# Optimization experiments

Hardware: AMD Instinct MI355X
Metric: run time of the kernel (lower is better)

## Reference

```python
import jax, jax.numpy as jnp
import numpy as np

B, T, HID = 2, 2048, 2048
H, KVH, D = 16, 4, 128
N_REP = H // KVH


def _rotate_half(x):
    x1, x2 = jnp.split(x, 2, axis=-1)
    return jnp.concatenate([-x2, x1], axis=-1)


def setup_inputs() -> dict:
    key = jax.random.key(0)
    ks = jax.random.split(key, 8)
    hidden_states = jax.random.normal(ks[0], (B, T, HID), dtype=jnp.float32)
    # RoPE tables: standard theta=10000 frequencies, emb = cat(freqs, freqs)
    inv_freq = 1.0 / (10000.0 ** (np.arange(0, D, 2, dtype=np.float32) / D))
    pos = np.arange(T, dtype=np.float32)
    freqs = np.outer(pos, inv_freq)                      # [T, D/2]
    emb = np.concatenate([freqs, freqs], axis=-1)        # [T, D]
    cos = jnp.broadcast_to(jnp.cos(emb)[None], (B, T, D)).astype(jnp.float32)
    sin = jnp.broadcast_to(jnp.sin(emb)[None], (B, T, D)).astype(jnp.float32)
    # causal additive mask [1,1,T,T]
    neg = jnp.finfo(jnp.float32).min
    causal = jnp.where(jnp.tril(jnp.ones((T, T), dtype=bool)), 0.0, neg)
    attention_mask = causal[None, None].astype(jnp.float32)
    s = 0.02
    Wq = jax.random.normal(ks[1], (H * D, HID), dtype=jnp.float32) * s
    Wk = jax.random.normal(ks[2], (KVH * D, HID), dtype=jnp.float32) * s
    Wv = jax.random.normal(ks[3], (KVH * D, HID), dtype=jnp.float32) * s
    Wo = jax.random.normal(ks[4], (HID, H * D), dtype=jnp.float32) * s
    bq = jnp.zeros((H * D,), dtype=jnp.float32)
    bk = jnp.zeros((KVH * D,), dtype=jnp.float32)
    bv = jnp.zeros((KVH * D,), dtype=jnp.float32)
    return {"hidden_states": hidden_states, "cos": cos, "sin": sin,
            "attention_mask": attention_mask,
            "Wq": Wq, "bq": bq, "Wk": Wk, "bk": bk, "Wv": Wv, "bv": bv, "Wo": Wo}


def reference(hidden_states, cos, sin, attention_mask, Wq, bq, Wk, bk, Wv, bv, Wo):
    bsz, q_len, _ = hidden_states.shape
    q = (jnp.einsum('bth,oh->bto', hidden_states, Wq) + bq).reshape(bsz, q_len, H, D).transpose(0, 2, 1, 3)
    k = (jnp.einsum('bth,oh->bto', hidden_states, Wk) + bk).reshape(bsz, q_len, KVH, D).transpose(0, 2, 1, 3)
    v = (jnp.einsum('bth,oh->bto', hidden_states, Wv) + bv).reshape(bsz, q_len, KVH, D).transpose(0, 2, 1, 3)
    c = cos[:, None, :, :]  # [B,1,T,D]
    s = sin[:, None, :, :]
    q = q * c + _rotate_half(q) * s
    k = k * c + _rotate_half(k) * s
    # repeat KV heads to match Q heads (GQA)
    k = jnp.repeat(k, N_REP, axis=1)  # [B,H,T,D]
    v = jnp.repeat(v, N_REP, axis=1)
    scores = jnp.einsum('bhqd,bhkd->bhqk', q, k) / jnp.sqrt(jnp.float32(D))
    scores = scores + attention_mask
    attn = jax.nn.softmax(scores.astype(jnp.float32), axis=-1).astype(q.dtype)
    out = jnp.einsum('bhqk,bhkd->bhqd', attn, v)          # [B,H,T,D]
    out = out.transpose(0, 2, 1, 3).reshape(bsz, q_len, H * D)
    return jnp.einsum('bto,ho->bth', out, Wo)
```

## Files before the change

kernel.cpp:

```cpp
#include <hip/hip_runtime.h>
#include <hip/hip_bf16.h>
#include <stdint.h>

#define B_ 2
#define T_ 2048
#define HID_ 2048
#define H_ 16
#define KVH_ 4
#define D_ 128

typedef __attribute__((ext_vector_type(8))) short short8;
typedef __attribute__((ext_vector_type(4))) float f32x4;

__device__ __forceinline__ uint16_t f2bf(float x) {
  union { float f; uint32_t u; } c; c.f = x;
  uint32_t r = c.u + 0x7fffu + ((c.u >> 16) & 1u);
  return (uint16_t)(r >> 16);
}
__device__ __forceinline__ float bf2f(uint16_t b) {
  union { uint32_t u; float f; } c; c.u = ((uint32_t)b) << 16;
  return c.f;
}
__device__ __forceinline__ uint16_t hwbf(float x) {
  __hip_bfloat16 h = __float2bfloat16(x);
  return *reinterpret_cast<uint16_t*>(&h);
}

#define XM(r) (((r) & 7) ^ (((r) >> 1) & 4))
#define SC_Q 0.1275523865396698f

__global__ __launch_bounds__(256) void cvt_all(const float* __restrict__ hidden,
                                               const float* __restrict__ Wq,
                                               const float* __restrict__ Wk,
                                               const float* __restrict__ Wv,
                                               const float* __restrict__ Wo,
                                               const float* __restrict__ bq,
                                               const float* __restrict__ bk,
                                               const float* __restrict__ bv,
                                               uint16_t* __restrict__ hidb,
                                               uint16_t* __restrict__ wqkv,
                                               uint16_t* __restrict__ wob,
                                               float* __restrict__ biasq) {
  const int gtid = blockIdx.x * 256 + threadIdx.x;
  const int i = gtid * 4;
  const float* src;
  uint16_t* dst;
  if (i < 8388608)       { src = hidden + i;            dst = hidb + i; }
  else if (i < 12582912) { src = Wq + (i - 8388608);    dst = wqkv + (i - 8388608); }
  else if (i < 13631488) { src = Wk + (i - 12582912);   dst = wqkv + 4194304 + (i - 12582912); }
  else if (i < 14680064) { src = Wv + (i - 13631488);   dst = wqkv + 5242880 + (i - 13631488); }
  else                   { src = Wo + (i - 14680064);   dst = wob + (i - 14680064); }
  const float4 v = *reinterpret_cast<const float4*>(src);
  union { uint16_t s[4]; uint2 u; } pk;
  pk.s[0] = f2bf(v.x); pk.s[1] = f2bf(v.y); pk.s[2] = f2bf(v.z); pk.s[3] = f2bf(v.w);
  *reinterpret_cast<uint2*>(dst) = pk.u;
  if (gtid < 3072)
    biasq[gtid] = (gtid < 2048) ? bq[gtid] : (gtid < 2560) ? bk[gtid - 2048] : bv[gtid - 2560];
}

#define QBM 256
#define QBN 256
#define BK 64

__global__ __launch_bounds__(512, 2) void gemm_qkv(const uint16_t* __restrict__ A,
                                                   const uint16_t* __restrict__ Bt,
                                                   const float* __restrict__ bias,
                                                   const float* __restrict__ cosp,
                                                   const float* __restrict__ sinp,
                                                   uint16_t* __restrict__ Qo,
                                                   uint16_t* __restrict__ Ko,
                                                   uint16_t* __restrict__ VtG) {
  __shared__ __align__(16) uint16_t Al[2][QBM * BK];
  __shared__ __align__(16) uint16_t Bl[2][QBN * BK];
  const int K = 2048;
  const int tid = threadIdx.x;
  const int w = tid >> 6;
  const int lane = tid & 63;
  const int wr = w >> 2, wc = w & 3;
  const int lm = lane & 15, lg = lane >> 4;

  const int orig = blockIdx.y * gridDim.x + blockIdx.x;
  const int xcd = orig & 7;
  const int cc = orig >> 3;
  const int bm = ((xcd & 3) * 4 + (cc & 3)) * QBM;
  const int bn = ((xcd >> 2) * 6 + (cc >> 2)) * QBN;

  const int cb0 = (wc >> 1) * 128 + (wc & 1) * 32;
  const int colb[4] = {cb0, cb0 + 16, cb0 + 64, cb0 + 80};

  f32x4 acc[8][4];
  const f32x4 z4 = {0.f, 0.f, 0.f, 0.f};
#pragma unroll
  for (int i = 0; i < 8; ++i)
#pragma unroll
    for (int j = 0; j < 4; ++j) acc[i][j] = z4;

  const int nt = K >> 6;

  auto stage = [&](int b, int t) {
    const int k0 = t * BK;
#pragma unroll
    for (int it = 0; it < 4; ++it) {
      const int chunk = it * 512 + tid;
      const int r = chunk >> 3, c8 = chunk & 7;
      const int csw = (c8 ^ XM(r)) * 8;
      const uint16_t* gA = A + (size_t)(bm + r) * K + k0 + csw;
      const uint16_t* gB = Bt + (size_t)(bn + r) * K + k0 + csw;
      __builtin_amdgcn_global_load_lds((const __attribute__((address_space(1))) unsigned int*)gA,
                                       (__attribute__((address_space(3))) unsigned int*)(&Al[b][0] + chunk * 8),
                                       16, 0, 0);
      __builtin_amdgcn_global_load_lds((const __attribute__((address_space(1))) unsigned int*)gB,
                                       (__attribute__((address_space(3))) unsigned int*)(&Bl[b][0] + chunk * 8),
                                       16, 0, 0);
    }
  };

  stage(0, 0);
  __syncthreads();

  int cur = 0;
  for (int t = 0; t < nt; ++t) {
    if (t + 1 < nt) stage(cur ^ 1, t + 1);
#pragma unroll
    for (int kk = 0; kk < 2; ++kk) {
      short8 bfr[4];
#pragma unroll
      for (int ni = 0; ni < 4; ++ni) {
        const int rb = colb[ni] + lm;
        bfr[ni] = *reinterpret_cast<const short8*>(&Bl[cur][rb * BK + (((kk * 4 + lg) ^ XM(rb)) * 8)]);
      }
#pragma unroll
      for (int mi = 0; mi < 8; ++mi) {
        const int r = wr * 128 + mi * 16 + lm;
        const short8 af = *reinterpret_cast<const short8*>(&Al[cur][r * BK + (((kk * 4 + lg) ^ XM(r)) * 8)]);
#pragma unroll
        for (int ni = 0; ni < 4; ++ni)
          acc[mi][ni] = __builtin_amdgcn_mfma_f32_16x16x32_bf16(af, bfr[ni], acc[mi][ni], 0, 0, 0);
      }
    }
    __syncthreads();
    cur ^= 1;
  }

  float bb[4];
#pragma unroll
  for (int ni = 0; ni < 4; ++ni) bb[ni] = bias[bn + colb[ni] + lm];

  if (bn < 2560) {
    const bool isQ = (bn < 2048);
    const int head0 = (isQ ? (bn >> 7) : ((bn - 2048) >> 7)) + (wc >> 1);
    const int nh = isQ ? H_ : KVH_;
    uint16_t* dst = isQ ? Qo : Ko;
    const float sc = isQ ? SC_Q : 1.0f;
#pragma unroll
    for (int mi = 0; mi < 8; ++mi) {
#pragma unroll
      for (int r = 0; r < 4; ++r) {
        const int row = bm + wr * 128 + mi * 16 + lg * 4 + r;
        const int b = row >> 11, tt = row & 2047;
        const float* cr = cosp + ((size_t)b * T_ + tt) * D_;
        const float* sr = sinp + ((size_t)b * T_ + tt) * D_;
        uint16_t* drow = dst + (((size_t)(b * nh + head0)) * T_ + tt) * D_;
#pragma unroll
        for (int ni = 0; ni < 4; ++ni) {
          const int d = (wc & 1) * 32 + (ni & 1) * 16 + (ni >> 1) * 64 + lm;
          const float xv = acc[mi][ni][r] + bb[ni];
          const float pv = acc[mi][ni ^ 2][r] + bb[ni ^ 2];
          const float sgn = (ni < 2) ? -1.f : 1.f;
          drow[d] = f2bf((xv * cr[d] + sgn * pv * sr[d]) * sc);
        }
      }
    }
  } else {
    const int kvh = ((bn - 2560) >> 7) + (wc >> 1);
#pragma unroll
    for (int mi = 0; mi < 8; ++mi) {
      const int row0 = bm + wr * 128 + mi * 16 + lg * 4;
      const int b = row0 >> 11, t0 = row0 & 2047;
#pragma unroll
      for (int ni = 0; ni < 4; ++ni) {
        const int d = (wc & 1) * 32 + (ni & 1) * 16 + (ni >> 1) * 64 + lm;
        union { uint16_t s[4]; uint2 u; } pk;
#pragma unroll
        for (int r = 0; r < 4; ++r) pk.s[r] = f2bf(acc[mi][ni][r] + bb[ni]);
        *reinterpret_cast<uint2*>(VtG + ((size_t)(b * KVH_ + kvh) * D_ + d) * T_ + t0) = pk.u;
      }
    }
  }
}

#define BM 128
#define BN 128

__global__ __launch_bounds__(512, 4) void gemm_bt(const uint16_t* __restrict__ A,
                                                  const uint16_t* __restrict__ Bt,
                                                  float* __restrict__ Cv,
                                                  int M, int N, int K) {
  __shared__ __align__(16) uint16_t Al[2][BM * BK];
  __shared__ __align__(16) uint16_t Bl[2][BN * BK];
  const int tid = threadIdx.x;
  const int w = tid >> 6;
  const int lane = tid & 63;
  const int wr = w >> 1, wc = w & 1;
  const int lm = lane & 15, lg = lane >> 4;

  const int GX = gridDim.x;
  const int orig = blockIdx.y * GX + blockIdx.x;
  const int xcd = orig & 7;
  const int cc = orig >> 3;
  const int bm = ((xcd >> 1) * 8 + (cc & 7)) * BM;
  const int bn = ((xcd & 1) * (GX >> 1) + (cc >> 3)) * BN;

  f32x4 acc[2][4];
  const f32x4 z4 = {0.f, 0.f, 0.f, 0.f};
#pragma unroll
  for (int i = 0; i < 2; ++i)
#pragma unroll
    for (int j = 0; j < 4; ++j) acc[i][j] = z4;

  const int nt = K >> 6;

  auto stage = [&](int b, int t) {
    const int k0 = t * BK;
#pragma unroll
    for (int it = 0; it < 2; ++it) {
      const int chunk = it * 512 + tid;
      const int r = chunk >> 3, c8 = chunk & 7;
      const int csw = (c8 ^ XM(r)) * 8;
      const uint16_t* gA = A + (size_t)(bm + r) * K + k0 + csw;
      const uint16_t* gB = Bt + (size_t)(bn + r) * K + k0 + csw;
      __builtin_amdgcn_global_load_lds((const __attribute__((address_space(1))) unsigned int*)gA,
                                       (__attribute__((address_space(3))) unsigned int*)(&Al[b][0] + chunk * 8),
                                       16, 0, 0);
      __builtin_amdgcn_global_load_lds((const __attribute__((address_space(1))) unsigned int*)gB,
                                       (__attribute__((address_space(3))) unsigned int*)(&Bl[b][0] + chunk * 8),
                                       16, 0, 0);
    }
  };

  stage(0, 0);
  __syncthreads();

  int cur = 0;
  for (int t = 0; t < nt; ++t) {
    if (t + 1 < nt) stage(cur ^ 1, t + 1);
#pragma unroll
    for (int kk = 0; kk < 2; ++kk) {
      short8 af[2], bfr[4];
#pragma unroll
      for (int mi = 0; mi < 2; ++mi) {
        const int r = wr * 32 + mi * 16 + lm;
        af[mi] = *reinterpret_cast<const short8*>(&Al[cur][r * BK + (((kk * 4 + lg) ^ XM(r)) * 8)]);
      }
#pragma unroll
      for (int ni = 0; ni < 4; ++ni) {
        const int r = wc * 64 + ni * 16 + lm;
        bfr[ni] = *reinterpret_cast<const short8*>(&Bl[cur][r * BK + (((kk * 4 + lg) ^ XM(r)) * 8)]);
      }
#pragma unroll
      for (int mi = 0; mi < 2; ++mi)
#pragma unroll
        for (int ni = 0; ni < 4; ++ni)
          acc[mi][ni] = __builtin_amdgcn_mfma_f32_16x16x32_bf16(af[mi], bfr[ni], acc[mi][ni], 0, 0, 0);
    }
    __syncthreads();
    cur ^= 1;
  }

#pragma unroll
  for (int mi = 0; mi < 2; ++mi) {
#pragma unroll
    for (int ni = 0; ni < 4; ++ni) {
      const int col = bn + wc * 64 + ni * 16 + lm;
#pragma unroll
      for (int r = 0; r < 4; ++r) {
        const int row = bm + wr * 32 + mi * 16 + lg * 4 + r;
        Cv[(size_t)row * N + col] = acc[mi][ni][r];
      }
    }
  }
}

#define KVBLK 64

__global__ __launch_bounds__(256, 2) void attn_fwd(const uint16_t* __restrict__ Qb,
                                                   const uint16_t* __restrict__ Kb,
                                                   const uint16_t* __restrict__ VtG,
                                                   uint16_t* __restrict__ Ab) {
  __shared__ __align__(16) uint16_t Kl[2][KVBLK * D_];
  __shared__ __align__(16) uint16_t Vtl[2][D_ * KVBLK];
  __shared__ __align__(16) uint16_t Pl[4 * 16 * 64];
  const int tid = threadIdx.x;
  const int w = tid >> 6, lane = tid & 63;
  const int lm = lane & 15, lg = lane >> 4;
  const int bh = blockIdx.y;
  const int b = bh >> 4, h = bh & 15;
  const int kvh = h >> 2;
  const int qtA = (blockIdx.x + bh) & 15;
  const int qtB = 31 - qtA;
  const int nA = qtA + 1;
  const int ntot = 33;

  const uint16_t* Kbase = Kb + ((size_t)(b * KVH_ + kvh)) * T_ * D_;
  const uint16_t* Vtbase = VtG + ((size_t)(b * KVH_ + kvh)) * D_ * T_;
  uint16_t* Pw = Pl + w * 16 * 64;
  const f32x4 z4 = {0.f, 0.f, 0.f, 0.f};

  short8 vone;
#pragma unroll
  for (int j = 0; j < 8; ++j) vone[j] = (short)0x3F80;

  f32x4 o[8];
  f32x4 osum;
  float mrow[4];
  short8 qf[4];

  auto loadQ = [&](int qt) {
    const uint16_t* Qw = Qb + (((size_t)(b * H_ + h)) * T_ + qt * 64 + w * 16) * D_;
#pragma unroll
    for (int kk = 0; kk < 4; ++kk)
      qf[kk] = *reinterpret_cast<const short8*>(Qw + (size_t)lm * D_ + kk * 32 + lg * 8);
  };
  auto resetAcc = [&]() {
#pragma unroll
    for (int f = 0; f < 8; ++f) o[f] = z4;
    osum = z4;
#pragma unroll
    for (int r = 0; r < 4; ++r) mrow[r] = -1e30f;
  };
  auto flush = [&](int qt) {
    const int wr0 = qt * 64 + w * 16;
    float rcp[4];
#pragma unroll
    for (int r = 0; r < 4; ++r) rcp[r] = 1.0f / osum[r];
#pragma unroll
    for (int f = 0; f < 8; ++f) {
      const int col = h * D_ + f * 16 + lm;
#pragma unroll
      for (int r = 0; r < 4; ++r) {
        const int trow = wr0 + lg * 4 + r;
        Ab[((size_t)(b * T_ + trow)) * (H_ * D_) + col] = f2bf(o[f][r] * rcp[r]);
      }
    }
  };
  auto stage = [&](int buf, int kv0) {
#pragma unroll
    for (int it = 0; it < 4; ++it) {
      const int chunk = it * 256 + tid;
      {
        const int r = chunk >> 4, c16 = chunk & 15;
        const uint16_t* g = Kbase + (size_t)(kv0 + r) * D_ + ((c16 ^ XM(r)) * 8);
        __builtin_amdgcn_global_load_lds((const __attribute__((address_space(1))) unsigned int*)g,
                                         (__attribute__((address_space(3))) unsigned int*)(&Kl[buf][0] + (it * 256 + w * 64) * 8),
                                         16, 0, 0);
      }
      {
        const int dd = chunk >> 3, c8 = chunk & 7;
        const uint16_t* g = Vtbase + (size_t)dd * T_ + kv0 + ((c8 ^ XM(dd)) * 8);
        __builtin_amdgcn_global_load_lds((const __attribute__((address_space(1))) unsigned int*)g,
                                         (__attribute__((address_space(3))) unsigned int*)(&Vtl[buf][0] + (it * 256 + w * 64) * 8),
                                         16, 0, 0);
      }
    }
  };

  loadQ(qtA);
  resetAcc();
  stage(0, 0);
  __syncthreads();

  int cur = 0;
  for (int g = 0; g < ntot; ++g) {
    const bool inA = g < nA;
    const int t = inA ? g : g - nA;
    const int qt = inA ? qtA : qtB;
    const int kv0 = t * KVBLK;
    const int wrow0 = qt * 64 + w * 16;

    if (g + 1 < ntot) {
      const int gn = g + 1;
      const int kvn = (gn < nA ? gn : gn - nA) * KVBLK;
      stage(cur ^ 1, kvn);
    }

    f32x4 s[4];
#pragma unroll
    for (int nf = 0; nf < 4; ++nf) s[nf] = z4;
#pragma unroll
    for (int nf = 0; nf < 4; ++nf)
#pragma unroll
      for (int kk = 0; kk < 4; ++kk) {
        const int row = nf * 16 + lm;
        const short8 kf = *reinterpret_cast<const short8*>(&Kl[cur][row * D_ + (((kk * 4 + lg) ^ XM(row)) * 8)]);
        s[nf] = __builtin_amdgcn_mfma_f32_16x16x32_bf16(qf[kk], kf, s[nf], 0, 0, 0);
      }

    if (kv0 + KVBLK - 1 > wrow0) {
#pragma unroll
      for (int nf = 0; nf < 4; ++nf) {
        const int colg = kv0 + nf * 16 + lm;
#pragma unroll
        for (int r = 0; r < 4; ++r) {
          const int rowg = wrow0 + lg * 4 + r;
          if (colg > rowg) s[nf][r] = -1e30f;
        }
      }
    }

    float tmax[4];
#pragma unroll
    for (int r = 0; r < 4; ++r)
      tmax[r] = fmaxf(fmaxf(s[0][r], s[1][r]), fmaxf(s[2][r], s[3][r]));
    bool grow = false;
#pragma unroll
    for (int r = 0; r < 4; ++r) grow = grow || (tmax[r] > mrow[r] + 8.f);
    if (__any((int)grow)) {
#pragma unroll
      for (int r = 0; r < 4; ++r) {
        float v = tmax[r];
        v = fmaxf(v, __shfl_xor(v, 1));
        v = fmaxf(v, __shfl_xor(v, 2));
        v = fmaxf(v, __shfl_xor(v, 4));
        v = fmaxf(v, __shfl_xor(v, 8));
        const float nm = fmaxf(mrow[r], v);
        const float al = exp2f(mrow[r] - nm);
        mrow[r] = nm;
        osum[r] *= al;
#pragma unroll
        for (int f = 0; f < 8; ++f) o[f][r] *= al;
      }
    }
#pragma unroll
    for (int nf = 0; nf < 4; ++nf)
#pragma unroll
      for (int r = 0; r < 4; ++r) {
        const float p = exp2f(s[nf][r] - mrow[r]);
        const int prow = lg * 4 + r;
        const int pchunk = (nf * 2 + (lm >> 3)) ^ XM(prow);
        Pw[prow * 64 + pchunk * 8 + (lm & 7)] = hwbf(p);
      }
    asm volatile("s_waitcnt lgkmcnt(0)" ::: "memory");
    short8 pf[2];
#pragma unroll
    for (int ks = 0; ks < 2; ++ks)
      pf[ks] = *reinterpret_cast<const short8*>(Pw + lm * 64 + (((ks * 4 + lg) ^ XM(lm)) * 8));
#pragma unroll
    for (int ks = 0; ks < 2; ++ks)
      osum = __builtin_amdgcn_mfma_f32_16x16x32_bf16(pf[ks], vone, osum, 0, 0, 0);
#pragma unroll
    for (int f = 0; f < 8; ++f)
#pragma unroll
      for (int ks = 0; ks < 2; ++ks) {
        const int dd = f * 16 + lm;
        const short8 vf = *reinterpret_cast<const short8*>(&Vtl[cur][dd * KVBLK + (((ks * 4 + lg) ^ XM(dd)) * 8)]);
        o[f] = __builtin_amdgcn_mfma_f32_16x16x32_bf16(pf[ks], vf, o[f], 0, 0, 0);
      }

    __syncthreads();
    cur ^= 1;

    if (g == nA - 1) {
      flush(qtA);
      loadQ(qtB);
      resetAcc();
    }
  }
  flush(qtB);
}

extern "C" void kernel_launch(void* const* d_in, const int* in_sizes, int n_in,
                              void* d_out, int out_size, void* d_ws, size_t ws_size,
                              hipStream_t stream) {
  const float* hidden = (const float*)d_in[0];
  const float* cosp   = (const float*)d_in[1];
  const float* sinp   = (const float*)d_in[2];
  const float* Wq = (const float*)d_in[4];
  const float* bq = (const float*)d_in[5];
  const float* Wk = (const float*)d_in[6];
  const float* bk = (const float*)d_in[7];
  const float* Wv = (const float*)d_in[8];
  const float* bv = (const float*)d_in[9];
  const float* Wo = (const float*)d_in[10];

  char* ws = (char*)d_ws;
  uint16_t* hidb   = (uint16_t*)(ws);
  uint16_t* wqkv   = (uint16_t*)(ws + 16777216);
  uint16_t* wob    = (uint16_t*)(ws + 29360128);
  float*    biasq  = (float*)   (ws + 37748736);
  uint16_t* Qb     = (uint16_t*)(ws + 62926848);
  uint16_t* Kb     = (uint16_t*)(ws + 79704064);
  uint16_t* VtG    = (uint16_t*)(ws + 83898368);
  uint16_t* Ab     = (uint16_t*)(ws + 88092672);

  cvt_all<<<18432, 256, 0, stream>>>(hidden, Wq, Wk, Wv, Wo, bq, bk, bv,
                                     hidb, wqkv, wob, biasq);
  gemm_qkv<<<dim3(12, 16), 512, 0, stream>>>(hidb, wqkv, biasq, cosp, sinp, Qb, Kb, VtG);
  attn_fwd<<<dim3(16, 32), 256, 0, stream>>>(Qb, Kb, VtG, Ab);
  gemm_bt<<<dim3(16, 32), 512, 0, stream>>>(Ab, wob, (float*)d_out, 4096, 2048, 2048);
}
```

Measured before the change: 200.3 us.

## Restructure QKV GEMM into 8-phase quadrant pipeline with half-tile staged loads

```diff
diff --git a/kernel.cpp b/kernel.cpp
--- a/kernel.cpp
+++ b/kernel.cpp
@@ -76,7 +76,7 @@
   const int tid = threadIdx.x;
   const int w = tid >> 6;
   const int lane = tid & 63;
-  const int wr = w >> 2, wc = w & 3;
+  const int wr = w >> 1, wc = w & 1;
   const int lm = lane & 15, lg = lane >> 4;
 
   const int orig = blockIdx.y * gridDim.x + blockIdx.x;
@@ -85,105 +85,153 @@
   const int bm = ((xcd & 3) * 4 + (cc & 3)) * QBM;
   const int bn = ((xcd >> 2) * 6 + (cc >> 2)) * QBN;
 
-  const int cb0 = (wc >> 1) * 128 + (wc & 1) * 32;
-  const int colb[4] = {cb0, cb0 + 16, cb0 + 64, cb0 + 80};
-
-  f32x4 acc[8][4];
+  f32x4 acc[4][2][4];
   const f32x4 z4 = {0.f, 0.f, 0.f, 0.f};
 #pragma unroll
-  for (int i = 0; i < 8; ++i)
-#pragma unroll
-    for (int j = 0; j < 4; ++j) acc[i][j] = z4;
-
-  const int nt = K >> 6;
-
-  auto stage = [&](int b, int t) {
+  for (int q = 0; q < 4; ++q)
+#pragma unroll
+    for (int mi = 0; mi < 2; ++mi)
+#pragma unroll
+      for (int ni = 0; ni < 4; ++ni) acc[q][mi][ni] = z4;
+
+  auto stage_half = [&](int buf, int t, int mat, int hh) {
     const int k0 = t * BK;
 #pragma unroll
-    for (int it = 0; it < 4; ++it) {
+    for (int it = 0; it < 2; ++it) {
       const int chunk = it * 512 + tid;
       const int r = chunk >> 3, c8 = chunk & 7;
-      const int csw = (c8 ^ XM(r)) * 8;
-      const uint16_t* gA = A + (size_t)(bm + r) * K + k0 + csw;
-      const uint16_t* gB = Bt + (size_t)(bn + r) * K + k0 + csw;
-      __builtin_amdgcn_global_load_lds((const __attribute__((address_space(1))) unsigned int*)gA,
-                                       (__attribute__((address_space(3))) unsigned int*)(&Al[b][0] + chunk * 8),
+      const int rr = hh * 128 + r;
+      const int csw = (c8 ^ XM(rr)) * 8;
+      const uint16_t* g = (mat == 0) ? (A + (size_t)(bm + rr) * K + k0 + csw)
+                                     : (Bt + (size_t)(bn + rr) * K + k0 + csw);
+      uint16_t* lb = (mat == 0) ? &Al[buf][0] : &Bl[buf][0];
+      __builtin_amdgcn_global_load_lds((const __attribute__((address_space(1))) unsigned int*)g,
+                                       (__attribute__((address_space(3))) unsigned int*)(lb + (size_t)rr * BK + c8 * 8),
                                        16, 0, 0);
-      __builtin_amdgcn_global_load_lds((const __attribute__((address_space(1))) unsigned int*)gB,
-                                       (__attribute__((address_space(3))) unsigned int*)(&Bl[b][0] + chunk * 8),
-                                       16, 0, 0);
     }
   };
 
-  stage(0, 0);
-  __syncthreads();
-
-  int cur = 0;
-  for (int t = 0; t < nt; ++t) {
-    if (t + 1 < nt) stage(cur ^ 1, t + 1);
-#pragma unroll
-    for (int kk = 0; kk < 2; ++kk) {
-      short8 bfr[4];
-#pragma unroll
-      for (int ni = 0; ni < 4; ++ni) {
-        const int rb = colb[ni] + lm;
-        bfr[ni] = *reinterpret_cast<const short8*>(&Bl[cur][rb * BK + (((kk * 4 + lg) ^ XM(rb)) * 8)]);
-      }
-#pragma unroll
-      for (int mi = 0; mi < 8; ++mi) {
-        const int r = wr * 128 + mi * 16 + lm;
-        const short8 af = *reinterpret_cast<const short8*>(&Al[cur][r * BK + (((kk * 4 + lg) ^ XM(r)) * 8)]);
-#pragma unroll
-        for (int ni = 0; ni < 4; ++ni)
-          acc[mi][ni] = __builtin_amdgcn_mfma_f32_16x16x32_bf16(af, bfr[ni], acc[mi][ni], 0, 0, 0);
-      }
-    }
-    __syncthreads();
-    cur ^= 1;
+  stage_half(0, 0, 1, 0);
+  stage_half(0, 0, 0, 0);
+  stage_half(0, 0, 0, 1);
+  stage_half(0, 0, 1, 1);
+  stage_half(1, 1, 1, 0);
+  stage_half(1, 1, 0, 0);
+  asm volatile("s_waitcnt vmcnt(8)" ::: "memory");
+  __builtin_amdgcn_s_barrier();
+
+  const int nIter = 16;
+  for (int i = 0; i < nIter; ++i) {
+    const bool lastIt = (i == nIter - 1);
+#pragma unroll
+    for (int p = 0; p < 8; ++p) {
+      const int bufc = p >> 2;
+      const int q = p & 3;
+      const int mh = q & 1, nh = q >> 1;
+      short8 af[2][2], bf[4][2];
+#pragma unroll
+      for (int mi = 0; mi < 2; ++mi)
+#pragma unroll
+        for (int kk = 0; kk < 2; ++kk) {
+          const int row = mh * 128 + wr * 32 + mi * 16 + lm;
+          af[mi][kk] = *reinterpret_cast<const short8*>(&Al[bufc][(size_t)row * BK + (((kk * 4 + lg) ^ XM(row)) * 8)]);
+        }
+#pragma unroll
+      for (int ni = 0; ni < 4; ++ni)
+#pragma unroll
+        for (int kk = 0; kk < 2; ++kk) {
+          const int row = nh * 128 + wc * 32 + (ni & 1) * 16 + (ni >> 1) * 64 + lm;
+          bf[ni][kk] = *reinterpret_cast<const short8*>(&Bl[bufc][(size_t)row * BK + (((kk * 4 + lg) ^ XM(row)) * 8)]);
+        }
+      if (p == 0)      stage_half(1, 2 * i + 1, 0, 1);
+      else if (p == 1) stage_half(1, 2 * i + 1, 1, 1);
+      else if (!lastIt) {
+        if (p == 2)      stage_half(0, 2 * i + 2, 1, 0);
+        else if (p == 3) stage_half(0, 2 * i + 2, 0, 0);
+        else if (p == 4) stage_half(0, 2 * i + 2, 0, 1);
+        else if (p == 5) stage_half(0, 2 * i + 2, 1, 1);
+        else if (p == 6) stage_half(1, 2 * i + 3, 1, 0);
+        else             stage_half(1, 2 * i + 3, 0, 0);
+      }
+      __builtin_amdgcn_s_barrier();
+      asm volatile("s_waitcnt lgkmcnt(0)" ::: "memory");
+      __builtin_amdgcn_sched_barrier(0);
+      __builtin_amdgcn_s_setprio(1);
+#pragma unroll
+      for (int kk = 0; kk < 2; ++kk)
+#pragma unroll
+        for (int mi = 0; mi < 2; ++mi)
+#pragma unroll
+          for (int ni = 0; ni < 4; ++ni)
+            acc[q][mi][ni] = __builtin_amdgcn_mfma_f32_16x16x32_bf16(af[mi][kk], bf[ni][kk], acc[q][mi][ni], 0, 0, 0);
+      __builtin_amdgcn_s_setprio(0);
+      if (p == 3) {
+        if (lastIt) asm volatile("s_waitcnt vmcnt(0)" ::: "memory");
+        else        asm volatile("s_waitcnt vmcnt(8)" ::: "memory");
+      } else if (p == 0 || p == 1 || p == 4 || p == 5 || p == 7) {
+        asm volatile("s_waitcnt vmcnt(8)" ::: "memory");
+      }
+      __builtin_amdgcn_s_barrier();
+    }
   }
 
-  float bb[4];
-#pragma unroll
-  for (int ni = 0; ni < 4; ++ni) bb[ni] = bias[bn + colb[ni] + lm];
-
-  if (bn < 2560) {
-    const bool isQ = (bn < 2048);
-    const int head0 = (isQ ? (bn >> 7) : ((bn - 2048) >> 7)) + (wc >> 1);
-    const int nh = isQ ? H_ : KVH_;
-    uint16_t* dst = isQ ? Qo : Ko;
-    const float sc = isQ ? SC_Q : 1.0f;
-#pragma unroll
-    for (int mi = 0; mi < 8; ++mi) {
-#pragma unroll
-      for (int r = 0; r < 4; ++r) {
-        const int row = bm + wr * 128 + mi * 16 + lg * 4 + r;
-        const int b = row >> 11, tt = row & 2047;
-        const float* cr = cosp + ((size_t)b * T_ + tt) * D_;
-        const float* sr = sinp + ((size_t)b * T_ + tt) * D_;
-        uint16_t* drow = dst + (((size_t)(b * nh + head0)) * T_ + tt) * D_;
-#pragma unroll
-        for (int ni = 0; ni < 4; ++ni) {
-          const int d = (wc & 1) * 32 + (ni & 1) * 16 + (ni >> 1) * 64 + lm;
-          const float xv = acc[mi][ni][r] + bb[ni];
-          const float pv = acc[mi][ni ^ 2][r] + bb[ni ^ 2];
-          const float sgn = (ni < 2) ? -1.f : 1.f;
-          drow[d] = f2bf((xv * cr[d] + sgn * pv * sr[d]) * sc);
+  float bb[2][4];
+#pragma unroll
+  for (int nh = 0; nh < 2; ++nh)
+#pragma unroll
+    for (int ni = 0; ni < 4; ++ni)
+      bb[nh][ni] = bias[bn + nh * 128 + wc * 32 + (ni & 1) * 16 + (ni >> 1) * 64 + lm];
+
+#pragma unroll
+  for (int nh = 0; nh < 2; ++nh) {
+    const int nb = bn + nh * 128;
+    if (nb < 2560) {
+      const bool isQ = (nb < 2048);
+      const int head = isQ ? (nb >> 7) : ((nb - 2048) >> 7);
+      const int nhd = isQ ? H_ : KVH_;
+      uint16_t* dst = isQ ? Qo : Ko;
+      const float sc = isQ ? SC_Q : 1.0f;
+#pragma unroll
+      for (int mh = 0; mh < 2; ++mh) {
+        const int q = mh + 2 * nh;
+#pragma unroll
+        for (int mi = 0; mi < 2; ++mi) {
+#pragma unroll
+          for (int r = 0; r < 4; ++r) {
+            const int row = bm + mh * 128 + wr * 32 + mi * 16 + lg * 4 + r;
+            const int b = row >> 11, tt = row & 2047;
+            const float* cr = cosp + ((size_t)b * T_ + tt) * D_;
+            const float* sr = sinp + ((size_t)b * T_ + tt) * D_;
+            uint16_t* drow = dst + (((size_t)(b * nhd + head)) * T_ + tt) * D_;
+#pragma unroll
+            for (int ni = 0; ni < 4; ++ni) {
+              const int d = wc * 32 + (ni & 1) * 16 + (ni >> 1) * 64 + lm;
+              const float xv = acc[q][mi][ni][r] + bb[nh][ni];
+              const float pv = acc[q][mi][ni ^ 2][r] + bb[nh][ni ^ 2];
+              const float sgn = (ni < 2) ? -1.f : 1.f;
+              drow[d] = f2bf((xv * cr[d] + sgn * pv * sr[d]) * sc);
+            }
+          }
         }
       }
-    }
-  } else {
-    const int kvh = ((bn - 2560) >> 7) + (wc >> 1);
-#pragma unroll
-    for (int mi = 0; mi < 8; ++mi) {
-      const int row0 = bm + wr * 128 + mi * 16 + lg * 4;
-      const int b = row0 >> 11, t0 = row0 & 2047;
-#pragma unroll
-      for (int ni = 0; ni < 4; ++ni) {
-        const int d = (wc & 1) * 32 + (ni & 1) * 16 + (ni >> 1) * 64 + lm;
-        union { uint16_t s[4]; uint2 u; } pk;
-#pragma unroll
-        for (int r = 0; r < 4; ++r) pk.s[r] = f2bf(acc[mi][ni][r] + bb[ni]);
-        *reinterpret_cast<uint2*>(VtG + ((size_t)(b * KVH_ + kvh) * D_ + d) * T_ + t0) = pk.u;
+    } else {
+      const int kvh = (nb - 2560) >> 7;
+#pragma unroll
+      for (int mh = 0; mh < 2; ++mh) {
+        const int q = mh + 2 * nh;
+#pragma unroll
+        for (int mi = 0; mi < 2; ++mi) {
+          const int row0 = bm + mh * 128 + wr * 32 + mi * 16 + lg * 4;
+          const int b = row0 >> 11, t0 = row0 & 2047;
+#pragma unroll
+          for (int ni = 0; ni < 4; ++ni) {
+            const int d = wc * 32 + (ni & 1) * 16 + (ni >> 1) * 64 + lm;
+            union { uint16_t s[4]; uint2 u; } pk;
+#pragma unroll
+            for (int r = 0; r < 4; ++r) pk.s[r] = f2bf(acc[q][mi][ni][r] + bb[nh][ni]);
+            *reinterpret_cast<uint2*>(VtG + ((size_t)(b * KVH_ + kvh) * D_ + d) * T_ + t0) = pk.u;
+          }
+        }
       }
     }
   }
```

After: 223.4 us. 11.5% more time.
